# Kernel optimization log

Hardware: AMD Instinct MI355X
Metric: run time of the kernel (lower is better)

The kernel has to match this reference:

```python
import jax, jax.numpy as jnp
import numpy as np

N = 50000   # number of nodes (= net_old.shape[0] = n_actions)
E = 1600000 # number of directed edges (avg degree 32)
HID = 128


def _gcn_conv(h, row, col, n, W, b):
    """PyG GCNConv: h' = D^-1/2 (A+I) D^-1/2 (h W) + b.
    row/col already include self loops. Aggregation is at the `col` (target) index."""
    h = h @ W  # [n, hid]
    deg = jax.ops.segment_sum(jnp.ones_like(col, dtype=h.dtype), col, num_segments=n)
    dinv = jnp.where(deg > 0, jax.lax.rsqrt(jnp.maximum(deg, 1e-12)), 0.0)
    norm = dinv[row] * dinv[col]                       # [e]
    msg = h[row] * norm[:, None]                       # [e, hid] gather (memory bound)
    return jax.ops.segment_sum(msg, col, num_segments=n) + b


def setup_inputs() -> dict:
    key = jax.random.key(0)
    ks = jax.random.split(key, 20)
    s3 = 1.0 / np.sqrt(3.0)
    sh = 1.0 / np.sqrt(HID)
    s3h = 1.0 / np.sqrt(3.0 * HID)
    s2h = 1.0 / np.sqrt(2.0 * HID)
    inp = {
        "x": jax.random.normal(ks[0], (N, 3), dtype=jnp.float32),
        "edge_index": jax.random.randint(ks[1], (2, E), 0, N, dtype=jnp.int32),
        "action_sel": jax.random.randint(ks[2], (N,), 0, 2, dtype=jnp.int32),
        "w1": jax.random.uniform(ks[3], (3, HID), jnp.float32, -s3, s3),
        "b1": jax.random.uniform(ks[4], (HID,), jnp.float32, -s3, s3),
        "wc1": jax.random.uniform(ks[5], (HID, HID), jnp.float32, -sh, sh),
        "bc1": jax.random.uniform(ks[6], (HID,), jnp.float32, -sh, sh),
        "wc2": jax.random.uniform(ks[7], (HID, HID), jnp.float32, -sh, sh),
        "bc2": jax.random.uniform(ks[8], (HID,), jnp.float32, -sh, sh),
        "w2": jax.random.uniform(ks[9], (3 * HID, HID), jnp.float32, -s3h, s3h),
        "b2": jax.random.uniform(ks[10], (HID,), jnp.float32, -s3h, s3h),
        "w5": jax.random.uniform(ks[11], (2 * HID, HID), jnp.float32, -s2h, s2h),
        "b5": jax.random.uniform(ks[12], (HID,), jnp.float32, -s2h, s2h),
        "w6": jax.random.uniform(ks[13], (HID, HID), jnp.float32, -sh, sh),
        "b6": jax.random.uniform(ks[14], (HID,), jnp.float32, -sh, sh),
        "w8": jax.random.uniform(ks[15], (HID, 1), jnp.float32, -sh, sh),
        "b8": jax.random.uniform(ks[16], (1,), jnp.float32, -sh, sh),
    }
    return inp


def reference(x, edge_index, action_sel, w1, b1, wc1, bc1, wc2, bc2,
              w2, b2, w5, b5, w6, b6, w8, b8):
    n = x.shape[0]
    # GCNConv adds self loops by default
    self_idx = jnp.arange(n, dtype=edge_index.dtype)
    row = jnp.concatenate([edge_index[0], self_idx])
    col = jnp.concatenate([edge_index[1], self_idx])

    x1 = x @ w1 + b1                                       # lin1: [N, hid]
    x2 = jax.nn.relu(_gcn_conv(x1, row, col, n, wc1, bc1)) # conv1 + relu
    x3 = jax.nn.relu(_gcn_conv(x2, row, col, n, wc2, bc2)) # conv2 + relu
    nodes_vec = jnp.concatenate([x1, x2, x3], axis=-1) @ w2 + b2  # lin2: [N, hid]

    # scatter_add(nodes_vec, action_sel, dim=-2)[0] == sum of nodes with action_sel==0
    mask0 = (action_sel == 0).astype(nodes_vec.dtype)[:, None]
    pool0 = jnp.sum(nodes_vec * mask0, axis=0)             # [hid]
    g = pool0 @ w6 + b6                                    # lin6 of repeated pool (same row for all nodes)

    cat = jnp.concatenate([jnp.broadcast_to(g, (n, HID)), nodes_vec], axis=-1)  # [N, 2*hid]
    h = jax.nn.relu(jax.nn.relu(cat) @ w5 + b5)            # lin5
    q = (h @ w8 + b8).squeeze(-1)                          # lin8 -> [N]
    return q, nodes_vec
```

## Files before the change

kernel.cpp:

```cpp
#include <hip/hip_runtime.h>

#define HID 128
#define CAP 8960
#define EPB 4096

typedef __attribute__((ext_vector_type(8))) short bf16x8;
typedef __attribute__((ext_vector_type(4))) float f32x4;
typedef __attribute__((ext_vector_type(2))) float f32x2;

__device__ __forceinline__ unsigned short f2bf(float f) {
  unsigned u = __builtin_bit_cast(unsigned, f);
  u += 0x7FFFu + ((u >> 16) & 1u);
  return (unsigned short)(u >> 16);
}
__device__ __forceinline__ float bflo(unsigned v) {
  return __builtin_bit_cast(float, v << 16);
}
__device__ __forceinline__ float bfhi(unsigned v) {
  return __builtin_bit_cast(float, v & 0xFFFF0000u);
}
__device__ __forceinline__ unsigned pck(float a, float b) {
  return (unsigned)f2bf(a) | ((unsigned)f2bf(b) << 16);
}


__global__ __launch_bounds__(256) void k_pre(
    const float* __restrict__ x, const float* __restrict__ w1, const float* __restrict__ b1,
    const float* __restrict__ wc1, const float* __restrict__ wc2,
    const float* __restrict__ w5b, const float* __restrict__ w2,
    unsigned short* __restrict__ wc1t, unsigned short* __restrict__ wc2t,
    unsigned short* __restrict__ w5bt, unsigned short* __restrict__ w2t,
    unsigned* __restrict__ x1,
    const int* __restrict__ erow, const int* __restrict__ ecol,
    int* __restrict__ gcnt, unsigned* __restrict__ ebuf, int e, int bgrid, int n) {
  __shared__ int hist[256], base[256], cur[256];
  int b = blockIdx.x;
  int tid = threadIdx.x;
  if (b < bgrid) {
    hist[tid] = 0;
    cur[tid] = 0;
    __syncthreads();
    int eb = b * EPB;
    int cc[16], rr[16];
#pragma unroll
    for (int k = 0; k < 16; ++k) {
      int i = eb + k * 256 + tid;
      if (i < e) {
        cc[k] = ecol[i];
        rr[k] = erow[i];
        atomicAdd(&hist[cc[k] >> 8], 1);
      } else {
        cc[k] = -1;
        rr[k] = 0;
      }
    }
    __syncthreads();
    if (hist[tid]) base[tid] = atomicAdd(&gcnt[tid], hist[tid]);
    __syncthreads();
#pragma unroll
    for (int k = 0; k < 16; ++k) {
      if (cc[k] >= 0) {
        int bk = cc[k] >> 8;
        int slot = base[bk] + atomicAdd(&cur[bk], 1);
        if (slot < CAP)
          ebuf[(size_t)bk * CAP + slot] = (unsigned)rr[k] | ((unsigned)(cc[k] & 255) << 16);
      }
    }
    return;
  }
  b -= bgrid;
  if (b < 384) {
    int idx = b * 256 + tid;
    if (idx < 16384) {
      int nn = idx >> 7, k = idx & 127;
      wc1t[idx] = f2bf(wc1[k * HID + nn]);
    } else if (idx < 32768) {
      int e2 = idx - 16384, nn = e2 >> 7, k = e2 & 127;
      wc2t[e2] = f2bf(wc2[k * HID + nn]);
    } else if (idx < 49152) {
      int e2 = idx - 32768, nn = e2 >> 7, k = e2 & 127;
      w5bt[e2] = f2bf(w5b[k * HID + nn]);
    } else if (idx < 98304) {
      int e2 = idx - 49152, nn = e2 / 384, k = e2 - nn * 384;
      w2t[e2] = f2bf(w2[k * HID + nn]);
    }
    return;
  }
  b -= 384;
  int idx = b * 256 + tid;
  if (idx >= n * 64) return;
  int i = idx >> 6, j = (idx & 63) * 2;
  float x0 = x[i * 3], xv1 = x[i * 3 + 1], xv2 = x[i * 3 + 2];
  float v0 = b1[j] + x0 * w1[j] + xv1 * w1[HID + j] + xv2 * w1[2 * HID + j];
  float v1 = b1[j + 1] + x0 * w1[j + 1] + xv1 * w1[HID + j + 1] + xv2 * w1[2 * HID + j + 1];
  x1[idx] = pck(v0, v1);
}


__device__ __forceinline__ void gconv_body(int bid, const unsigned short* __restrict__ A,
                                           const unsigned short* __restrict__ Bt,
                                           unsigned char* __restrict__ C, int n) {
  int tid = threadIdx.x, lane = tid & 63, wave = tid >> 6;
  int lm = lane & 15, lk = lane >> 4;
  int row0 = bid * 64 + (wave >> 1) * 32;
  int col0 = (wave & 1) * 64;
  int ra = min(row0 + lm, n - 1), rb = min(row0 + 16 + lm, n - 1);
  f32x4 acc[2][4] = {};
#pragma unroll
  for (int ks = 0; ks < 4; ++ks) {
    bf16x8 a0 = *reinterpret_cast<const bf16x8*>(A + (size_t)ra * HID + ks * 32 + lk * 8);
    bf16x8 a1 = *reinterpret_cast<const bf16x8*>(A + (size_t)rb * HID + ks * 32 + lk * 8);
#pragma unroll
    for (int ct = 0; ct < 4; ++ct) {
      bf16x8 bb = *reinterpret_cast<const bf16x8*>(Bt + (size_t)(col0 + ct * 16 + lm) * HID + ks * 32 + lk * 8);
      acc[0][ct] = __builtin_amdgcn_mfma_f32_16x16x32_bf16(a0, bb, acc[0][ct], 0, 0, 0);
      acc[1][ct] = __builtin_amdgcn_mfma_f32_16x16x32_bf16(a1, bb, acc[1][ct], 0, 0, 0);
    }
  }
#pragma unroll
  for (int rt = 0; rt < 2; ++rt)
#pragma unroll
    for (int r = 0; r < 4; ++r) {
      int row = row0 + rt * 16 + lk * 4 + r;
      if (row < n) {
        int pa = __builtin_amdgcn_cvt_pk_fp8_f32(acc[rt][0][r], acc[rt][1][r], 0, false);
        int pb = __builtin_amdgcn_cvt_pk_fp8_f32(acc[rt][2][r], acc[rt][3][r], 0, false);
        size_t base = (size_t)row * HID + col0 + lm;
        C[base]      = (unsigned char)(pa & 0xFF);
        C[base + 16] = (unsigned char)((pa >> 8) & 0xFF);
        C[base + 32] = (unsigned char)(pb & 0xFF);
        C[base + 48] = (unsigned char)((pb >> 8) & 0xFF);
      }
    }
}


__global__ __launch_bounds__(256) void k_csrconv(
    const unsigned* __restrict__ ebuf, const int* __restrict__ gcnt,
    unsigned short* __restrict__ csr, int* __restrict__ offg, int* __restrict__ cnt,
    float* __restrict__ dinv,
    const unsigned short* __restrict__ A, const unsigned short* __restrict__ Bt,
    unsigned char* __restrict__ C, int n, int nbkt) {
  __shared__ int hist[256], scan[256], cur[256];
  int tid = threadIdx.x, b = blockIdx.x;
  if (b < nbkt) {
    int m = min(gcnt[b], CAP);
    hist[tid] = 0;
    cur[tid] = 0;
    __syncthreads();
    const unsigned* eb = ebuf + (size_t)b * CAP;
    for (int i = tid; i < m; i += 256) atomicAdd(&hist[(eb[i] >> 16) & 255], 1);
    __syncthreads();
    scan[tid] = hist[tid];
    __syncthreads();
    for (int d = 1; d < 256; d <<= 1) {
      int t = (tid >= d) ? scan[tid - d] : 0;
      __syncthreads();
      scan[tid] += t;
      __syncthreads();
    }
    scan[tid] -= hist[tid];
    int c = b * 256 + tid;
    if (c < n) {
      cnt[c] = hist[tid];
      offg[c] = b * CAP + scan[tid];
      dinv[c] = rsqrtf((float)hist[tid] + 1.0f);
    }
    __syncthreads();
    unsigned short* cb = csr + (size_t)b * CAP;
    for (int i = tid; i < m; i += 256) {
      unsigned eg = eb[i];
      int lc = (eg >> 16) & 255;
      cb[scan[lc] + atomicAdd(&cur[lc], 1)] = (unsigned short)(eg & 0xFFFF);
    }
    return;
  }
  gconv_body(b - nbkt, A, Bt, C, n);
}

__global__ void k_gconv(const unsigned short* __restrict__ A,
                        const unsigned short* __restrict__ Bt,
                        unsigned char* __restrict__ C, int n) {
  gconv_body(blockIdx.x, A, Bt, C, n);
}


__global__ __launch_bounds__(256) void k_agg(const uint4* __restrict__ h,
                                             const float* __restrict__ dinv,
                                             const int* __restrict__ offg,
                                             const int* __restrict__ cnt,
                                             const unsigned short* __restrict__ csr,
                                             const float* __restrict__ bias,
                                             uint4* __restrict__ out, int n) {
  int wave = threadIdx.x >> 6, lane = threadIdx.x & 63;
  int c = blockIdx.x * 4 + wave;
  if (c >= n) return;
  int g = lane >> 3, cp = lane & 7;
  float dc = dinv[c];
  float acc[16];
  {
    uint4 v = h[(size_t)c * 8 + cp];
    float ws = (g == 0) ? dc : 0.f;
    f32x2 p;
    p = __builtin_amdgcn_cvt_pk_f32_fp8((int)v.x, false); acc[0] = p.x * ws; acc[1] = p.y * ws;
    p = __builtin_amdgcn_cvt_pk_f32_fp8((int)v.x, true);  acc[2] = p.x * ws; acc[3] = p.y * ws;
    p = __builtin_amdgcn_cvt_pk_f32_fp8((int)v.y, false); acc[4] = p.x * ws; acc[5] = p.y * ws;
    p = __builtin_amdgcn_cvt_pk_f32_fp8((int)v.y, true);  acc[6] = p.x * ws; acc[7] = p.y * ws;
    p = __builtin_amdgcn_cvt_pk_f32_fp8((int)v.z, false); acc[8] = p.x * ws; acc[9] = p.y * ws;
    p = __builtin_amdgcn_cvt_pk_f32_fp8((int)v.z, true);  acc[10] = p.x * ws; acc[11] = p.y * ws;
    p = __builtin_amdgcn_cvt_pk_f32_fp8((int)v.w, false); acc[12] = p.x * ws; acc[13] = p.y * ws;
    p = __builtin_amdgcn_cvt_pk_f32_fp8((int)v.w, true);  acc[14] = p.x * ws; acc[15] = p.y * ws;
  }
  int s = offg[c], t = s + cnt[c];
  for (int idx = s; idx < t; idx += 16) {
    int j0 = idx + g, j1 = idx + 8 + g;
    bool v0 = j0 < t, v1 = j1 < t;
    int r0 = csr[v0 ? j0 : s];
    int r1 = csr[v1 ? j1 : s];
    float w0 = v0 ? dinv[r0] : 0.f;
    float w1 = v1 ? dinv[r1] : 0.f;
    uint4 h0 = h[(size_t)r0 * 8 + cp];
    uint4 h1 = h[(size_t)r1 * 8 + cp];
    f32x2 p;
#define ACC8(vv, ww)                                                                     \
    p = __builtin_amdgcn_cvt_pk_f32_fp8((int)vv.x, false); acc[0] = fmaf(p.x, ww, acc[0]); acc[1] = fmaf(p.y, ww, acc[1]); \
    p = __builtin_amdgcn_cvt_pk_f32_fp8((int)vv.x, true);  acc[2] = fmaf(p.x, ww, acc[2]); acc[3] = fmaf(p.y, ww, acc[3]); \
    p = __builtin_amdgcn_cvt_pk_f32_fp8((int)vv.y, false); acc[4] = fmaf(p.x, ww, acc[4]); acc[5] = fmaf(p.y, ww, acc[5]); \
    p = __builtin_amdgcn_cvt_pk_f32_fp8((int)vv.y, true);  acc[6] = fmaf(p.x, ww, acc[6]); acc[7] = fmaf(p.y, ww, acc[7]); \
    p = __builtin_amdgcn_cvt_pk_f32_fp8((int)vv.z, false); acc[8] = fmaf(p.x, ww, acc[8]); acc[9] = fmaf(p.y, ww, acc[9]); \
    p = __builtin_amdgcn_cvt_pk_f32_fp8((int)vv.z, true);  acc[10] = fmaf(p.x, ww, acc[10]); acc[11] = fmaf(p.y, ww, acc[11]); \
    p = __builtin_amdgcn_cvt_pk_f32_fp8((int)vv.w, false); acc[12] = fmaf(p.x, ww, acc[12]); acc[13] = fmaf(p.y, ww, acc[13]); \
    p = __builtin_amdgcn_cvt_pk_f32_fp8((int)vv.w, true);  acc[14] = fmaf(p.x, ww, acc[14]); acc[15] = fmaf(p.y, ww, acc[15]);
    ACC8(h0, w0)
    ACC8(h1, w1)
#undef ACC8
  }
#pragma unroll
  for (int i = 0; i < 16; ++i) {
    acc[i] += __shfl_xor(acc[i], 8);
    acc[i] += __shfl_xor(acc[i], 16);
    acc[i] += __shfl_xor(acc[i], 32);
  }
  if (g == 0) {
    int cb = cp * 16;
    uint4 o1, o2;
    o1.x = pck(fmaxf(fmaf(acc[0], dc, bias[cb + 0]), 0.f), fmaxf(fmaf(acc[1], dc, bias[cb + 1]), 0.f));
    o1.y = pck(fmaxf(fmaf(acc[2], dc, bias[cb + 2]), 0.f), fmaxf(fmaf(acc[3], dc, bias[cb + 3]), 0.f));
    o1.z = pck(fmaxf(fmaf(acc[4], dc, bias[cb + 4]), 0.f), fmaxf(fmaf(acc[5], dc, bias[cb + 5]), 0.f));
    o1.w = pck(fmaxf(fmaf(acc[6], dc, bias[cb + 6]), 0.f), fmaxf(fmaf(acc[7], dc, bias[cb + 7]), 0.f));
    o2.x = pck(fmaxf(fmaf(acc[8], dc, bias[cb + 8]), 0.f), fmaxf(fmaf(acc[9], dc, bias[cb + 9]), 0.f));
    o2.y = pck(fmaxf(fmaf(acc[10], dc, bias[cb + 10]), 0.f), fmaxf(fmaf(acc[11], dc, bias[cb + 11]), 0.f));
    o2.z = pck(fmaxf(fmaf(acc[12], dc, bias[cb + 12]), 0.f), fmaxf(fmaf(acc[13], dc, bias[cb + 13]), 0.f));
    o2.w = pck(fmaxf(fmaf(acc[14], dc, bias[cb + 14]), 0.f), fmaxf(fmaf(acc[15], dc, bias[cb + 15]), 0.f));
    out[(size_t)c * 16 + cp * 2] = o1;
    out[(size_t)c * 16 + cp * 2 + 1] = o2;
  }
}


__global__ __launch_bounds__(256) void k_gnv(const unsigned short* __restrict__ A1,
                                             const unsigned short* __restrict__ A2,
                                             const unsigned short* __restrict__ A3,
                                             const unsigned short* __restrict__ Bt,
                                             const float* __restrict__ b2,
                                             const int* __restrict__ sel,
                                             float* __restrict__ nv,
                                             unsigned short* __restrict__ nvr,
                                             float* __restrict__ part, int n) {
  __shared__ float spart[HID];
  int tid = threadIdx.x, lane = tid & 63, wave = tid >> 6;
  if (tid < HID) spart[tid] = 0.f;
  int lm = lane & 15, lk = lane >> 4;
  int row0 = blockIdx.x * 64 + (wave >> 1) * 32;
  int col0 = (wave & 1) * 64;
  int ra = min(row0 + lm, n - 1), rb = min(row0 + 16 + lm, n - 1);
  f32x4 acc[2][4] = {};
  const unsigned short* As[3] = {A1, A2, A3};
#pragma unroll
  for (int kb = 0; kb < 3; ++kb) {
    const unsigned short* A = As[kb];
#pragma unroll
    for (int ks = 0; ks < 4; ++ks) {
      bf16x8 a0 = *reinterpret_cast<const bf16x8*>(A + (size_t)ra * HID + ks * 32 + lk * 8);
      bf16x8 a1 = *reinterpret_cast<const bf16x8*>(A + (size_t)rb * HID + ks * 32 + lk * 8);
#pragma unroll
      for (int ct = 0; ct < 4; ++ct) {
        bf16x8 bb = *reinterpret_cast<const bf16x8*>(
            Bt + (size_t)(col0 + ct * 16 + lm) * 384 + kb * 128 + ks * 32 + lk * 8);
        acc[0][ct] = __builtin_amdgcn_mfma_f32_16x16x32_bf16(a0, bb, acc[0][ct], 0, 0, 0);
        acc[1][ct] = __builtin_amdgcn_mfma_f32_16x16x32_bf16(a1, bb, acc[1][ct], 0, 0, 0);
      }
    }
  }
  float psum[4] = {0.f, 0.f, 0.f, 0.f};
#pragma unroll
  for (int rt = 0; rt < 2; ++rt)
#pragma unroll
    for (int r = 0; r < 4; ++r) {
      int row = row0 + rt * 16 + lk * 4 + r;
      if (row < n) {
        float m = (sel[row] == 0) ? 1.f : 0.f;
#pragma unroll
        for (int ct = 0; ct < 4; ++ct) {
          int col = col0 + ct * 16 + lm;
          float v = acc[rt][ct][r] + b2[col];
          nv[(size_t)row * HID + col] = v;
          nvr[(size_t)row * HID + col] = f2bf(fmaxf(v, 0.f));
          psum[ct] = fmaf(m, v, psum[ct]);
        }
      }
    }
#pragma unroll
  for (int ct = 0; ct < 4; ++ct) {
    psum[ct] += __shfl_xor(psum[ct], 16);
    psum[ct] += __shfl_xor(psum[ct], 32);
  }
  __syncthreads();
  if (lk == 0) {
#pragma unroll
    for (int ct = 0; ct < 4; ++ct) atomicAdd(&spart[col0 + ct * 16 + lm], psum[ct]);
  }
  __syncthreads();
  if (tid < HID) part[(size_t)blockIdx.x * HID + tid] = spart[tid];
}


__global__ __launch_bounds__(1024) void k_g(const float* __restrict__ part, int nblk,
                                            const float* __restrict__ w6, const float* __restrict__ b6,
                                            const float* __restrict__ w5, const float* __restrict__ b5,
                                            float* __restrict__ gb5) {
  __shared__ float red[8][HID];
  __shared__ float p0[HID], gl[HID];
  int t = threadIdx.x, j = t & 127, grp = t >> 7;
  float a0 = 0.f, a1 = 0.f, a2 = 0.f, a3 = 0.f;
  int r = grp;
  for (; r + 32 <= nblk; r += 32) {
    a0 += part[(size_t)(r)*HID + j];
    a1 += part[(size_t)(r + 8) * HID + j];
    a2 += part[(size_t)(r + 16) * HID + j];
    a3 += part[(size_t)(r + 24) * HID + j];
  }
  for (; r < nblk; r += 8) a0 += part[(size_t)r * HID + j];
  red[grp][j] = (a0 + a1) + (a2 + a3);
  __syncthreads();
  if (grp == 0)
    p0[j] = ((red[0][j] + red[1][j]) + (red[2][j] + red[3][j])) +
            ((red[4][j] + red[5][j]) + (red[6][j] + red[7][j]));
  __syncthreads();
  float acc = 0.f;
#pragma unroll
  for (int k = 0; k < 16; ++k) acc = fmaf(p0[grp * 16 + k], w6[(grp * 16 + k) * HID + j], acc);
  red[grp][j] = acc;
  __syncthreads();
  if (grp == 0) {
    float s = ((red[0][j] + red[1][j]) + (red[2][j] + red[3][j])) +
              ((red[4][j] + red[5][j]) + (red[6][j] + red[7][j])) + b6[j];
    gl[j] = fmaxf(s, 0.f);
  }
  __syncthreads();
  acc = 0.f;
#pragma unroll
  for (int k = 0; k < 16; ++k) acc = fmaf(gl[grp * 16 + k], w5[(grp * 16 + k) * HID + j], acc);
  red[grp][j] = acc;
  __syncthreads();
  if (grp == 0)
    gb5[j] = ((red[0][j] + red[1][j]) + (red[2][j] + red[3][j])) +
             ((red[4][j] + red[5][j]) + (red[6][j] + red[7][j])) + b5[j];
}


__global__ __launch_bounds__(256) void k_gq(const unsigned short* __restrict__ A,
                                            const unsigned short* __restrict__ Bt,
                                            const float* __restrict__ gb5,
                                            const float* __restrict__ w8,
                                            const float* __restrict__ b8,
                                            float* __restrict__ q, int n) {
  __shared__ float sq[2][64];
  int tid = threadIdx.x, lane = tid & 63, wave = tid >> 6;
  int lm = lane & 15, lk = lane >> 4;
  int row0 = blockIdx.x * 64 + (wave >> 1) * 32;
  int col0 = (wave & 1) * 64;
  int ra = min(row0 + lm, n - 1), rb = min(row0 + 16 + lm, n - 1);
  f32x4 acc[2][4] = {};
#pragma unroll
  for (int ks = 0; ks < 4; ++ks) {
    bf16x8 a0 = *reinterpret_cast<const bf16x8*>(A + (size_t)ra * HID + ks * 32 + lk * 8);
    bf16x8 a1 = *reinterpret_cast<const bf16x8*>(A + (size_t)rb * HID + ks * 32 + lk * 8);
#pragma unroll
    for (int ct = 0; ct < 4; ++ct) {
      bf16x8 bb = *reinterpret_cast<const bf16x8*>(Bt + (size_t)(col0 + ct * 16 + lm) * HID + ks * 32 + lk * 8);
      acc[0][ct] = __builtin_amdgcn_mfma_f32_16x16x32_bf16(a0, bb, acc[0][ct], 0, 0, 0);
      acc[1][ct] = __builtin_amdgcn_mfma_f32_16x16x32_bf16(a1, bb, acc[1][ct], 0, 0, 0);
    }
  }
  float ps[2][4];
#pragma unroll
  for (int rt = 0; rt < 2; ++rt)
#pragma unroll
    for (int r = 0; r < 4; ++r) {
      float p = 0.f;
#pragma unroll
      for (int ct = 0; ct < 4; ++ct) {
        int col = col0 + ct * 16 + lm;
        float v = fmaxf(acc[rt][ct][r] + gb5[col], 0.f);
        p = fmaf(v, w8[col], p);
      }
      ps[rt][r] = p;
    }
#pragma unroll
  for (int rt = 0; rt < 2; ++rt)
#pragma unroll
    for (int r = 0; r < 4; ++r) {
#pragma unroll
      for (int d = 1; d < 16; d <<= 1) ps[rt][r] += __shfl_xor(ps[rt][r], d);
    }
  if (lm == 0) {
#pragma unroll
    for (int rt = 0; rt < 2; ++rt)
#pragma unroll
      for (int r = 0; r < 4; ++r)
        sq[wave & 1][(wave >> 1) * 32 + rt * 16 + lk * 4 + r] = ps[rt][r];
  }
  __syncthreads();
  if (tid < 64) {
    int row = blockIdx.x * 64 + tid;
    if (row < n) q[row] = sq[0][tid] + sq[1][tid] + b8[0];
  }
}


extern "C" void kernel_launch(void* const* d_in, const int* in_sizes, int n_in,
                              void* d_out, int out_size, void* d_ws, size_t ws_size,
                              hipStream_t stream) {
  const float* x   = (const float*)d_in[0];
  const int*   ei  = (const int*)d_in[1];
  const int*   sel = (const int*)d_in[2];
  const float* w1  = (const float*)d_in[3];
  const float* b1  = (const float*)d_in[4];
  const float* wc1 = (const float*)d_in[5];
  const float* bc1 = (const float*)d_in[6];
  const float* wc2 = (const float*)d_in[7];
  const float* bc2 = (const float*)d_in[8];
  const float* w2  = (const float*)d_in[9];
  const float* b2  = (const float*)d_in[10];
  const float* w5  = (const float*)d_in[11];
  const float* b5  = (const float*)d_in[12];
  const float* w6  = (const float*)d_in[13];
  const float* b6  = (const float*)d_in[14];
  const float* w8  = (const float*)d_in[15];
  const float* b8  = (const float*)d_in[16];

  int n = in_sizes[0] / 3;
  int e = in_sizes[1] / 2;
  const int* erow = ei;
  const int* ecol = ei + e;

  float* q  = (float*)d_out;
  float* nv = q + n;

  int ggrid = (n + 63) / 64;
  int lgrid = (n * 64 + 255) / 256;
  int nbkt  = (n + 255) >> 8;
  int bgrid = (e + EPB - 1) / EPB;

  unsigned short* x1b = (unsigned short*)d_ws;
  unsigned short* x2b = x1b + (size_t)n * HID;
  unsigned short* x3b = x2b + (size_t)n * HID;
  unsigned char*  hb  = (unsigned char*)(x3b + (size_t)n * HID);
  unsigned short* nvr = (unsigned short*)(hb + (size_t)n * HID);
  unsigned short* wc1t = nvr + (size_t)n * HID;
  unsigned short* wc2t = wc1t + HID * HID;
  unsigned short* w5bt = wc2t + HID * HID;
  unsigned short* w2t  = w5bt + HID * HID;
  float* fw = (float*)(w2t + 384 * HID);
  float* dinv  = fw; fw += n;
  float* part  = fw; fw += (size_t)ggrid * HID;
  float* gb5   = fw; fw += HID;
  int* iw = (int*)fw;
  int* gcnt = iw; iw += 256;
  int* offg = iw; iw += n;
  int* cnt  = iw; iw += n;
  unsigned* ebuf = (unsigned*)iw; iw += (size_t)nbkt * CAP;
  unsigned short* csr = (unsigned short*)iw;

  hipMemsetAsync(gcnt, 0, 256 * sizeof(int), stream);
  k_pre<<<bgrid + 384 + lgrid, 256, 0, stream>>>(x, w1, b1, wc1, wc2, w5 + HID * HID, w2,
                                                 wc1t, wc2t, w5bt, w2t, (unsigned*)x1b,
                                                 erow, ecol, gcnt, ebuf, e, bgrid, n);
  k_csrconv<<<nbkt + ggrid, 256, 0, stream>>>(ebuf, gcnt, csr, offg, cnt, dinv,
                                              x1b, wc1t, hb, n, nbkt);
  k_agg<<<(n + 3) / 4, 256, 0, stream>>>((const uint4*)hb, dinv, offg, cnt, csr, bc1, (uint4*)x2b, n);
  k_gconv<<<ggrid, 256, 0, stream>>>(x2b, wc2t, hb, n);
  k_agg<<<(n + 3) / 4, 256, 0, stream>>>((const uint4*)hb, dinv, offg, cnt, csr, bc2, (uint4*)x3b, n);
  k_gnv<<<ggrid, 256, 0, stream>>>(x1b, x2b, x3b, w2t, b2, sel, nv, nvr, part, n);
  k_g<<<1, 1024, 0, stream>>>(part, ggrid, w6, b6, w5, b5, gb5);
  k_gq<<<ggrid, 256, 0, stream>>>(nvr, w5bt, gb5, w8, b8, q, n);
}
```

Measured before the change: 229.5 us.

## Unroll aggregation gathers 4-way, widen CSR indices, fold global reduction into last block

The aggregation loop now handles 32 neighbors per iteration, issuing four independent index and row gathers before accumulating, to keep more memory loads in flight. CSR indices are stored as 32-bit ints instead of 16-bit, which doubles index traffic but gives simpler aligned loads. The separate single-block reduction kernel is removed: the last block of k_gnv, found with an atomic counter and threadfence, sums the partials and computes the w6/w5 vectors. This saves one launch, but that final reduction now runs on 256 threads instead of 1024.

```diff
diff --git a/kernel.cpp b/kernel.cpp
--- a/kernel.cpp
+++ b/kernel.cpp
@@ -137,7 +137,7 @@
 
 __global__ __launch_bounds__(256) void k_csrconv(
     const unsigned* __restrict__ ebuf, const int* __restrict__ gcnt,
-    unsigned short* __restrict__ csr, int* __restrict__ offg, int* __restrict__ cnt,
+    int* __restrict__ csr, int* __restrict__ offg, int* __restrict__ cnt,
     float* __restrict__ dinv,
     const unsigned short* __restrict__ A, const unsigned short* __restrict__ Bt,
     unsigned char* __restrict__ C, int n, int nbkt) {
@@ -167,11 +167,11 @@
       dinv[c] = rsqrtf((float)hist[tid] + 1.0f);
     }
     __syncthreads();
-    unsigned short* cb = csr + (size_t)b * CAP;
+    int* cb = csr + (size_t)b * CAP;
     for (int i = tid; i < m; i += 256) {
       unsigned eg = eb[i];
       int lc = (eg >> 16) & 255;
-      cb[scan[lc] + atomicAdd(&cur[lc], 1)] = (unsigned short)(eg & 0xFFFF);
+      cb[scan[lc] + atomicAdd(&cur[lc], 1)] = (int)(eg & 0xFFFF);
     }
     return;
   }
@@ -189,7 +189,7 @@
                                              const float* __restrict__ dinv,
                                              const int* __restrict__ offg,
                                              const int* __restrict__ cnt,
-                                             const unsigned short* __restrict__ csr,
+                                             const int* __restrict__ csr,
                                              const float* __restrict__ bias,
                                              uint4* __restrict__ out, int n) {
   int wave = threadIdx.x >> 6, lane = threadIdx.x & 63;
@@ -212,15 +212,19 @@
     p = __builtin_amdgcn_cvt_pk_f32_fp8((int)v.w, true);  acc[14] = p.x * ws; acc[15] = p.y * ws;
   }
   int s = offg[c], t = s + cnt[c];
-  for (int idx = s; idx < t; idx += 16) {
-    int j0 = idx + g, j1 = idx + 8 + g;
-    bool v0 = j0 < t, v1 = j1 < t;
-    int r0 = csr[v0 ? j0 : s];
-    int r1 = csr[v1 ? j1 : s];
-    float w0 = v0 ? dinv[r0] : 0.f;
-    float w1 = v1 ? dinv[r1] : 0.f;
-    uint4 h0 = h[(size_t)r0 * 8 + cp];
-    uint4 h1 = h[(size_t)r1 * 8 + cp];
+  for (int idx = s; idx < t; idx += 32) {
+    int r[4];
+    float w[4];
+#pragma unroll
+    for (int u = 0; u < 4; ++u) {
+      int j = idx + u * 8 + g;
+      bool vl = j < t;
+      r[u] = csr[vl ? j : s];
+      w[u] = vl ? dinv[r[u]] : 0.f;
+    }
+    uint4 hv[4];
+#pragma unroll
+    for (int u = 0; u < 4; ++u) hv[u] = h[(size_t)r[u] * 8 + cp];
     f32x2 p;
 #define ACC8(vv, ww)                                                                     \
     p = __builtin_amdgcn_cvt_pk_f32_fp8((int)vv.x, false); acc[0] = fmaf(p.x, ww, acc[0]); acc[1] = fmaf(p.y, ww, acc[1]); \
@@ -231,8 +235,10 @@
     p = __builtin_amdgcn_cvt_pk_f32_fp8((int)vv.z, true);  acc[10] = fmaf(p.x, ww, acc[10]); acc[11] = fmaf(p.y, ww, acc[11]); \
     p = __builtin_amdgcn_cvt_pk_f32_fp8((int)vv.w, false); acc[12] = fmaf(p.x, ww, acc[12]); acc[13] = fmaf(p.y, ww, acc[13]); \
     p = __builtin_amdgcn_cvt_pk_f32_fp8((int)vv.w, true);  acc[14] = fmaf(p.x, ww, acc[14]); acc[15] = fmaf(p.y, ww, acc[15]);
-    ACC8(h0, w0)
-    ACC8(h1, w1)
+    ACC8(hv[0], w[0])
+    ACC8(hv[1], w[1])
+    ACC8(hv[2], w[2])
+    ACC8(hv[3], w[3])
 #undef ACC8
   }
 #pragma unroll
@@ -266,7 +272,13 @@
                                              const int* __restrict__ sel,
                                              float* __restrict__ nv,
                                              unsigned short* __restrict__ nvr,
-                                             float* __restrict__ part, int n) {
+                                             float* __restrict__ part,
+                                             int* __restrict__ done,
+                                             const float* __restrict__ w6,
+                                             const float* __restrict__ b6,
+                                             const float* __restrict__ w5a,
+                                             const float* __restrict__ b5,
+                                             float* __restrict__ gb5, int n) {
   __shared__ float spart[HID];
   int tid = threadIdx.x, lane = tid & 63, wave = tid >> 6;
   if (tid < HID) spart[tid] = 0.f;
@@ -322,50 +334,41 @@
   }
   __syncthreads();
   if (tid < HID) part[(size_t)blockIdx.x * HID + tid] = spart[tid];
-}
-
-
-__global__ __launch_bounds__(1024) void k_g(const float* __restrict__ part, int nblk,
-                                            const float* __restrict__ w6, const float* __restrict__ b6,
-                                            const float* __restrict__ w5, const float* __restrict__ b5,
-                                            float* __restrict__ gb5) {
-  __shared__ float red[8][HID];
-  __shared__ float p0[HID], gl[HID];
-  int t = threadIdx.x, j = t & 127, grp = t >> 7;
+
+  __threadfence();
+  __shared__ int lastf;
+  if (tid == 0) lastf = (atomicAdd(done, 1) == (int)gridDim.x - 1) ? 1 : 0;
+  __syncthreads();
+  if (!lastf) return;
+  __shared__ float red[2][HID], p0[HID], gl[HID];
+  int j = tid & 127, grp = tid >> 7;
+  int nblk = gridDim.x;
   float a0 = 0.f, a1 = 0.f, a2 = 0.f, a3 = 0.f;
-  int r = grp;
-  for (; r + 32 <= nblk; r += 32) {
-    a0 += part[(size_t)(r)*HID + j];
-    a1 += part[(size_t)(r + 8) * HID + j];
-    a2 += part[(size_t)(r + 16) * HID + j];
-    a3 += part[(size_t)(r + 24) * HID + j];
-  }
-  for (; r < nblk; r += 8) a0 += part[(size_t)r * HID + j];
+  int r2 = grp;
+  for (; r2 + 8 <= nblk; r2 += 8) {
+    a0 += part[(size_t)(r2)*HID + j];
+    a1 += part[(size_t)(r2 + 2) * HID + j];
+    a2 += part[(size_t)(r2 + 4) * HID + j];
+    a3 += part[(size_t)(r2 + 6) * HID + j];
+  }
+  for (; r2 < nblk; r2 += 2) a0 += part[(size_t)r2 * HID + j];
   red[grp][j] = (a0 + a1) + (a2 + a3);
   __syncthreads();
-  if (grp == 0)
-    p0[j] = ((red[0][j] + red[1][j]) + (red[2][j] + red[3][j])) +
-            ((red[4][j] + red[5][j]) + (red[6][j] + red[7][j]));
-  __syncthreads();
-  float acc = 0.f;
-#pragma unroll
-  for (int k = 0; k < 16; ++k) acc = fmaf(p0[grp * 16 + k], w6[(grp * 16 + k) * HID + j], acc);
-  red[grp][j] = acc;
-  __syncthreads();
-  if (grp == 0) {
-    float s = ((red[0][j] + red[1][j]) + (red[2][j] + red[3][j])) +
-              ((red[4][j] + red[5][j]) + (red[6][j] + red[7][j])) + b6[j];
-    gl[j] = fmaxf(s, 0.f);
-  }
-  __syncthreads();
-  acc = 0.f;
-#pragma unroll
-  for (int k = 0; k < 16; ++k) acc = fmaf(gl[grp * 16 + k], w5[(grp * 16 + k) * HID + j], acc);
-  red[grp][j] = acc;
-  __syncthreads();
-  if (grp == 0)
-    gb5[j] = ((red[0][j] + red[1][j]) + (red[2][j] + red[3][j])) +
-             ((red[4][j] + red[5][j]) + (red[6][j] + red[7][j])) + b5[j];
+  if (grp == 0) p0[j] = red[0][j] + red[1][j];
+  __syncthreads();
+  float ac = 0.f;
+#pragma unroll 8
+  for (int k = 0; k < 64; ++k) ac = fmaf(p0[grp * 64 + k], w6[(grp * 64 + k) * HID + j], ac);
+  red[grp][j] = ac;
+  __syncthreads();
+  if (grp == 0) gl[j] = fmaxf(red[0][j] + red[1][j] + b6[j], 0.f);
+  __syncthreads();
+  ac = 0.f;
+#pragma unroll 8
+  for (int k = 0; k < 64; ++k) ac = fmaf(gl[grp * 64 + k], w5a[(grp * 64 + k) * HID + j], ac);
+  red[grp][j] = ac;
+  __syncthreads();
+  if (grp == 0) gb5[j] = red[0][j] + red[1][j] + b5[j];
 }
 
 
@@ -478,12 +481,13 @@
   float* gb5   = fw; fw += HID;
   int* iw = (int*)fw;
   int* gcnt = iw; iw += 256;
+  int* done = iw; iw += 1;
   int* offg = iw; iw += n;
   int* cnt  = iw; iw += n;
   unsigned* ebuf = (unsigned*)iw; iw += (size_t)nbkt * CAP;
-  unsigned short* csr = (unsigned short*)iw;
-
-  hipMemsetAsync(gcnt, 0, 256 * sizeof(int), stream);
+  int* csr = iw;
+
+  hipMemsetAsync(gcnt, 0, 257 * sizeof(int), stream);
   k_pre<<<bgrid + 384 + lgrid, 256, 0, stream>>>(x, w1, b1, wc1, wc2, w5 + HID * HID, w2,
                                                  wc1t, wc2t, w5bt, w2t, (unsigned*)x1b,
                                                  erow, ecol, gcnt, ebuf, e, bgrid, n);
@@ -492,7 +496,7 @@
   k_agg<<<(n + 3) / 4, 256, 0, stream>>>((const uint4*)hb, dinv, offg, cnt, csr, bc1, (uint4*)x2b, n);
   k_gconv<<<ggrid, 256, 0, stream>>>(x2b, wc2t, hb, n);
   k_agg<<<(n + 3) / 4, 256, 0, stream>>>((const uint4*)hb, dinv, offg, cnt, csr, bc2, (uint4*)x3b, n);
-  k_gnv<<<ggrid, 256, 0, stream>>>(x1b, x2b, x3b, w2t, b2, sel, nv, nvr, part, n);
-  k_g<<<1, 1024, 0, stream>>>(part, ggrid, w6, b6, w5, b5, gb5);
+  k_gnv<<<ggrid, 256, 0, stream>>>(x1b, x2b, x3b, w2t, b2, sel, nv, nvr, part,
+                                   done, w6, b6, w5, b5, gb5, n);
   k_gq<<<ggrid, 256, 0, stream>>>(nvr, w5bt, gb5, w8, b8, q, n);
 }
```

After: 369.4 us. +60.9%, slower.
